# Optimization experiments

Measured on AMD Instinct MI355X. Metric: run time of the kernel, lower is better.

## Reference

```python
import jax, jax.numpy as jnp
import numpy as np

N_NODES = 50000
N_EDGES = 800000
N_REL = 6
N_LAYERS = 8
D = 256
NUM_GRAPHS = 512


def setup_inputs() -> dict:
    key = jax.random.key(0)
    ks = jax.random.split(key, 24)
    s = lambda *sh: 1.0 / np.sqrt(sh[0])
    inp = {
        "x": jax.random.normal(ks[0], (N_NODES, 13), dtype=jnp.float32),
        "edge_index": jax.random.randint(ks[1], (2, N_EDGES), 0, N_NODES, dtype=jnp.int64),
        "edge_type": jax.random.randint(ks[2], (N_EDGES,), 0, N_REL, dtype=jnp.int64),
        "batch": jnp.sort(jax.random.randint(ks[3], (N_NODES,), 0, NUM_GRAPHS, dtype=jnp.int64)),
        "enc_W": jax.random.normal(ks[4], (13, D), dtype=jnp.float32) * s(13),
        "enc_b": jnp.zeros((D,), dtype=jnp.float32),
        "prelu_a": jnp.float32(0.25),
        "rel_W": jax.random.normal(ks[5], (N_LAYERS, N_REL, D, D), dtype=jnp.float32) * s(D),
        "root_W": jax.random.normal(ks[6], (N_LAYERS, D, D), dtype=jnp.float32) * s(D),
        "conv_b": jnp.zeros((N_LAYERS, D), dtype=jnp.float32),
        "gp_W1": jax.random.normal(ks[7], (D, D), dtype=jnp.float32) * s(D),
        "gp_b1": jnp.zeros((D,), dtype=jnp.float32),
        "gp_W2": jax.random.normal(ks[8], (D, D), dtype=jnp.float32) * s(D),
        "gp_b2": jnp.zeros((D,), dtype=jnp.float32),
        "fc_W1": jax.random.normal(ks[9], (D, 1024), dtype=jnp.float32) * s(D),
        "fc_b1": jnp.zeros((1024,), dtype=jnp.float32),
        "fc_W2": jax.random.normal(ks[10], (1024, 512), dtype=jnp.float32) * s(1024),
        "fc_b2": jnp.zeros((512,), dtype=jnp.float32),
        "out_W": jax.random.normal(ks[11], (512, 1), dtype=jnp.float32) * s(512),
        "out_b": jnp.zeros((1,), dtype=jnp.float32),
    }
    return inp


def reference(x, edge_index, edge_type, batch, enc_W, enc_b, prelu_a, rel_W, root_W,
              conv_b, gp_W1, gp_b1, gp_W2, gp_b2, fc_W1, fc_b1, fc_W2, fc_b2, out_W, out_b):
    src, dst = edge_index[0], edge_index[1]
    h = x @ enc_W + enc_b  # [N, D]
    for i in range(N_LAYERS):
        skip = h
        # per-relation transform for all nodes: [R, N, D]
        xW = jnp.einsum('nd,rde->rne', h, rel_W[i])
        msgs = xW[edge_type, src]  # [E, D] gather by (relation, source node)
        agg = jax.ops.segment_sum(msgs, dst, num_segments=N_NODES)
        h = agg + h @ root_W[i] + conv_b[i]
        h = h + skip
        h = jnp.where(h > 0, h, prelu_a * h)  # PReLU (shared scalar)
        norm = jnp.sqrt(jnp.sum(h * h, axis=1, keepdims=True))
        h = h / jnp.maximum(norm, 1e-12)  # F.normalize(p=2, dim=1)
    g = jax.nn.relu(h @ gp_W1 + gp_b1) @ gp_W2 + gp_b2
    pooled = jax.ops.segment_sum(g, batch, num_segments=NUM_GRAPHS)  # global_add_pool
    z = jax.nn.relu(pooled @ fc_W1 + fc_b1)  # dropout = identity at eval
    z = jax.nn.relu(z @ fc_W2 + fc_b2)
    return jax.nn.relu(z @ out_W + out_b)  # [NUM_GRAPHS, 1]
```

## Files before the change

kernel.cpp:

```cpp
#include <hip/hip_runtime.h>

#define N_NODES   50000
#define N_EDGES   800000
#define N_REL     6
#define N_LAYERS  8
#define DD        256
#define NUM_GRAPHS 512

#define NKEYS      (N_REL * N_NODES)
#define SCAN_T     256
#define SCAN_E     8
#define SCAN_CHUNK (SCAN_T * SCAN_E)
#define SCAN_NB    ((NKEYS + SCAN_CHUNK - 1) / SCAN_CHUNK)

typedef _Float16 h4 __attribute__((ext_vector_type(4)));
typedef _Float16 h8 __attribute__((ext_vector_type(8)));
typedef float    f4 __attribute__((ext_vector_type(4)));

__device__ __forceinline__ void atomAddF(float* p, float v) { unsafeAtomicAdd(p, v); }

__device__ __forceinline__ void load_lds16(const void* g, void* l) {
    __builtin_amdgcn_global_load_lds(
        (const __attribute__((address_space(1))) uint32_t*)g,
        (__attribute__((address_space(3))) uint32_t*)l, 16, 0, 0);
}

__global__ __launch_bounds__(256) void enc_kernel(const float* __restrict__ x,
                                                  const float* __restrict__ W,
                                                  const float* __restrict__ b,
                                                  _Float16* __restrict__ Hhi,
                                                  _Float16* __restrict__ Hlo) {
    int n = blockIdx.x;
    int d = threadIdx.x;
    float s = b[d];
#pragma unroll
    for (int k = 0; k < 13; ++k) s = fmaf(x[n * 13 + k], W[k * 256 + d], s);
    const _Float16 hi = (_Float16)s;
    Hhi[(size_t)n * DD + d] = hi;
    Hlo[(size_t)n * DD + d] = (_Float16)(s - (float)hi);
}

__global__ __launch_bounds__(256) void wsplit_rel_kernel(const float* __restrict__ relW,
                                                         const float* __restrict__ rootW,
                                                         _Float16* __restrict__ wthi,
                                                         _Float16* __restrict__ wtlo) {
    const size_t id = (size_t)blockIdx.x * 256 + threadIdx.x;
    if (id >= (size_t)N_LAYERS * 7 * 256 * 256) return;
    const int k = (int)(id & 255);
    const int n = (int)((id >> 8) & 255);
    const int g = (int)((id >> 16) % 7);
    const int L = (int)((id >> 16) / 7);
    float w = (g < 6)
        ? relW[(((size_t)L * 6 + g) * 256 + k) * 256 + n]
        : rootW[((size_t)L * 256 + k) * 256 + n];
    if (g == 6 && k == n) w += 1.0f;
    const _Float16 hi = (_Float16)w;
    const size_t o = ((size_t)L * 256 + n) * 1792 + (size_t)g * 256 + k;
    wthi[o] = hi;
    wtlo[o] = (_Float16)(w - (float)hi);
}

__global__ __launch_bounds__(256) void wsplit_tr_kernel(const float* __restrict__ W,
                                                        _Float16* __restrict__ whi,
                                                        _Float16* __restrict__ wlo,
                                                        int K, int N) {
    const size_t id = (size_t)blockIdx.x * 256 + threadIdx.x;
    if (id >= (size_t)K * N) return;
    const int k = (int)(id % K), n = (int)(id / K);
    const float w = W[(size_t)k * N + n];
    const _Float16 hi = (_Float16)w;
    whi[(size_t)n * K + k] = hi;
    wlo[(size_t)n * K + k] = (_Float16)(w - (float)hi);
}

__global__ __launch_bounds__(256) void fsplit_kernel(const float* __restrict__ S,
                                                     _Float16* __restrict__ hi,
                                                     _Float16* __restrict__ lo, int total) {
    const int id = blockIdx.x * 256 + threadIdx.x;
    if (id >= total) return;
    const float v = S[id];
    const _Float16 h = (_Float16)v;
    hi[id] = h;
    lo[id] = (_Float16)(v - (float)h);
}

__global__ __launch_bounds__(256, 2) void layer_kernel(
    const _Float16* __restrict__ Hhi, const _Float16* __restrict__ Hlo,
    const _Float16* __restrict__ Bhi, const _Float16* __restrict__ Blo,
    const int* __restrict__ ioff, const int* __restrict__ isrc,
    _Float16* __restrict__ Hnhi, _Float16* __restrict__ Hnlo,
    const float* __restrict__ bias, const float* __restrict__ pa) {
    __shared__ _Float16 smem[24576];
    const int tid  = threadIdx.x;
    const int lane = tid & 63;
    const int wave = tid >> 6;
    const int lm = lane & 15, lq = lane >> 4;
    const int wm = wave & 1, wn = wave >> 1;
    const int mb = blockIdx.x * 128;

    const int nl   = tid >> 1;
    const int half = tid & 1;
    const int node = min(mb + nl, N_NODES - 1);

    f4 acc[4][8];
#pragma unroll
    for (int i = 0; i < 4; ++i)
#pragma unroll
        for (int j = 0; j < 8; ++j) acc[i][j] = (f4){0.f, 0.f, 0.f, 0.f};

    for (int seg = 0; seg < 7; ++seg) {
        const bool isrel = (seg < 6);
        int s0 = 0, s1 = 0;
        if (isrel) {
            s0 = ioff[seg * N_NODES + node];
            s1 = ioff[seg * N_NODES + node + 1];
        }
#pragma unroll 1
        for (int c8 = 0; c8 < 8; ++c8) {
            const int acol = c8 * 32;
            const int bcol = seg * 256 + acol;

            __syncthreads();

            if (isrel) {
                float afp[16];
#pragma unroll
                for (int j = 0; j < 16; ++j) afp[j] = 0.f;
                const int dbase = acol + half * 16;
                for (int e = s0; e < s1; ++e) {
                    const int s = isrc[e];
                    const size_t hb = (size_t)s * DD + dbase;
                    const h8 vh0 = *(const h8*)(Hhi + hb);
                    const h8 vh1 = *(const h8*)(Hhi + hb + 8);
                    const h8 vl0 = *(const h8*)(Hlo + hb);
                    const h8 vl1 = *(const h8*)(Hlo + hb + 8);
#pragma unroll
                    for (int j = 0; j < 8; ++j) {
                        afp[j]     += (float)vh0[j] + (float)vl0[j];
                        afp[8 + j] += (float)vh1[j] + (float)vl1[j];
                    }
                }
#pragma unroll
                for (int u = 0; u < 2; ++u) {
                    h8 oh, ol;
#pragma unroll
                    for (int j = 0; j < 8; ++j) {
                        const float v = afp[u * 8 + j];
                        oh[j] = (_Float16)v;
                        ol[j] = (_Float16)(v - (float)oh[j]);
                    }
                    const int cc   = half * 2 + u;
                    const int slot = cc ^ ((nl >> 1) & 3);
                    const int o    = (nl * 4 + slot) * 8;
                    *(h8*)(smem + o)        = oh;
                    *(h8*)(smem + 4096 + o) = ol;
                }
#pragma unroll
                for (int q = 4; q < 12; ++q) {
                    const int ub = (q * 4 + wave) * 64;
                    const int u  = (ub + lane) & 1023;
                    const int row = u >> 2, slot = u & 3;
                    const int cx = slot ^ ((row >> 1) & 3);
                    const _Float16* gp = (q < 8) ? Bhi : Blo;
                    const size_t gb = (size_t)row * 1792 + bcol + cx * 8;
                    load_lds16(gp + gb, smem + (size_t)ub * 8);
                }
            } else {
#pragma unroll
                for (int q = 0; q < 12; ++q) {
                    const int ub = (q * 4 + wave) * 64;
                    const int u  = ub + lane;
                    const _Float16* gp;
                    size_t ga;
                    if (q < 4) {
                        const int v = u & 511, row = v >> 2, slot = v & 3;
                        const int cx = slot ^ ((row >> 1) & 3);
                        const int rg = min(mb + row, N_NODES - 1);
                        gp = (q < 2) ? Hhi : Hlo;
                        ga = (size_t)rg * DD + acol + cx * 8;
                    } else {
                        const int v = u & 1023, row = v >> 2, slot = v & 3;
                        const int cx = slot ^ ((row >> 1) & 3);
                        gp = (q < 8) ? Bhi : Blo;
                        ga = (size_t)row * 1792 + bcol + cx * 8;
                    }
                    load_lds16(gp + ga, smem + (size_t)ub * 8);
                }
            }
            __syncthreads();

            h8 ah[4], al[4], bh[8], bl[8];
#pragma unroll
            for (int i = 0; i < 4; ++i) {
                const int row  = wm * 64 + i * 16 + lm;
                const int slot = lq ^ ((row >> 1) & 3);
                const int o    = (row * 4 + slot) * 8;
                ah[i] = *(const h8*)(smem + o);
                al[i] = *(const h8*)(smem + 4096 + o);
            }
#pragma unroll
            for (int j = 0; j < 8; ++j) {
                const int n    = wn * 128 + j * 16 + lm;
                const int slot = lq ^ ((n >> 1) & 3);
                const int o    = (n * 4 + slot) * 8;
                bh[j] = *(const h8*)(smem + 8192 + o);
                bl[j] = *(const h8*)(smem + 16384 + o);
            }
#pragma unroll
            for (int i = 0; i < 4; ++i)
#pragma unroll
                for (int j = 0; j < 8; ++j) {
                    acc[i][j] = __builtin_amdgcn_mfma_f32_16x16x32_f16(ah[i], bh[j], acc[i][j], 0, 0, 0);
                    acc[i][j] = __builtin_amdgcn_mfma_f32_16x16x32_f16(ah[i], bl[j], acc[i][j], 0, 0, 0);
                    acc[i][j] = __builtin_amdgcn_mfma_f32_16x16x32_f16(al[i], bh[j], acc[i][j], 0, 0, 0);
                }
        }
    }

    float* shf = (float*)smem;
    const float a = pa[0];
    __syncthreads();
#pragma unroll
    for (int i = 0; i < 4; ++i)
#pragma unroll
        for (int r = 0; r < 4; ++r) {
            const int rl  = i * 16 + lq * 4 + r;
            const int row = mb + wm * 64 + rl;
            float rss = 0.f;
            if (row < N_NODES) {
#pragma unroll
                for (int j = 0; j < 8; ++j) {
                    const int col = wn * 128 + j * 16 + lm;
                    float v = acc[i][j][r] + bias[col];
                    v = v > 0.f ? v : a * v;
                    acc[i][j][r] = v;
                    rss = fmaf(v, v, rss);
                }
            }
            rss += __shfl_xor(rss, 1, 64);
            rss += __shfl_xor(rss, 2, 64);
            rss += __shfl_xor(rss, 4, 64);
            rss += __shfl_xor(rss, 8, 64);
            if (lm == 0 && row < N_NODES) shf[wave * 64 + rl] = rss;
        }
    __syncthreads();
#pragma unroll
    for (int i = 0; i < 4; ++i)
#pragma unroll
        for (int r = 0; r < 4; ++r) {
            const int rl  = i * 16 + lq * 4 + r;
            const int row = mb + wm * 64 + rl;
            if (row >= N_NODES) continue;
            const float tot = shf[wm * 64 + rl] + shf[(2 + wm) * 64 + rl];
            const float inv = 1.0f / fmaxf(sqrtf(tot), 1e-12f);
#pragma unroll
            for (int j = 0; j < 8; ++j) {
                const int col = wn * 128 + j * 16 + lm;
                const float v = acc[i][j][r] * inv;
                const _Float16 hi = (_Float16)v;
                const size_t idx = (size_t)row * DD + col;
                Hnhi[idx] = hi;
                Hnlo[idx] = (_Float16)(v - (float)hi);
            }
        }
}

template <int MODE>
__global__ __launch_bounds__(256, 2) void gemm_lds(
    const _Float16* __restrict__ Ahi, const _Float16* __restrict__ Alo,
    const _Float16* __restrict__ Bhi, const _Float16* __restrict__ Blo,
    int lda, int ldb, int ldc, int K_tot,
    _Float16* __restrict__ Ohi, _Float16* __restrict__ Olo,
    const float* __restrict__ bias, int M) {
    __shared__ _Float16 smem[24576];
    const int lane = threadIdx.x & 63;
    const int wave = threadIdx.x >> 6;
    const int lm = lane & 15, lq = lane >> 4;
    const int wm = wave & 1, wn = wave >> 1;
    const int mb = blockIdx.x * 128;
    const int nb = blockIdx.y * 256;

    f4 acc[4][8];
#pragma unroll
    for (int i = 0; i < 4; ++i)
#pragma unroll
        for (int j = 0; j < 8; ++j) acc[i][j] = (f4){0.f, 0.f, 0.f, 0.f};

    for (int k0 = 0; k0 < K_tot; k0 += 32) {
        __syncthreads();
#pragma unroll
        for (int q = 0; q < 12; ++q) {
            const int ub = (q * 4 + wave) * 64;
            const int u  = ub + lane;
            const _Float16* gp;
            size_t ga;
            if (q < 4) {
                const int v = u & 511, row = v >> 2, slot = v & 3;
                const int cx = slot ^ ((row >> 1) & 3);
                const int rg = min(mb + row, M - 1);
                gp = (q < 2) ? Ahi : Alo;
                ga = (size_t)rg * lda + k0 + cx * 8;
            } else {
                const int v = u & 1023, row = v >> 2, slot = v & 3;
                const int cx = slot ^ ((row >> 1) & 3);
                gp = (q < 8) ? Bhi : Blo;
                ga = (size_t)(nb + row) * ldb + k0 + cx * 8;
            }
            load_lds16(gp + ga, smem + (size_t)ub * 8);
        }
        __syncthreads();

        h8 ah[4], al[4], bh[8], bl[8];
#pragma unroll
        for (int i = 0; i < 4; ++i) {
            const int row  = wm * 64 + i * 16 + lm;
            const int slot = lq ^ ((row >> 1) & 3);
            const int o    = (row * 4 + slot) * 8;
            ah[i] = *(const h8*)(smem + o);
            al[i] = *(const h8*)(smem + 4096 + o);
        }
#pragma unroll
        for (int j = 0; j < 8; ++j) {
            const int n    = wn * 128 + j * 16 + lm;
            const int slot = lq ^ ((n >> 1) & 3);
            const int o    = (n * 4 + slot) * 8;
            bh[j] = *(const h8*)(smem + 8192 + o);
            bl[j] = *(const h8*)(smem + 16384 + o);
        }
#pragma unroll
        for (int i = 0; i < 4; ++i)
#pragma unroll
            for (int j = 0; j < 8; ++j) {
                acc[i][j] = __builtin_amdgcn_mfma_f32_16x16x32_f16(ah[i], bh[j], acc[i][j], 0, 0, 0);
                acc[i][j] = __builtin_amdgcn_mfma_f32_16x16x32_f16(ah[i], bl[j], acc[i][j], 0, 0, 0);
                acc[i][j] = __builtin_amdgcn_mfma_f32_16x16x32_f16(al[i], bh[j], acc[i][j], 0, 0, 0);
            }
    }

#pragma unroll
    for (int i = 0; i < 4; ++i)
#pragma unroll
        for (int r = 0; r < 4; ++r) {
            const int row = mb + wm * 64 + i * 16 + lq * 4 + r;
            if (row >= M) continue;
#pragma unroll
            for (int j = 0; j < 8; ++j) {
                const int col = nb + wn * 128 + j * 16 + lm;
                float v = acc[i][j][r] + bias[col];
                if (MODE == 2) v = fmaxf(v, 0.f);
                const _Float16 hi = (_Float16)v;
                const size_t idx = (size_t)row * ldc + col;
                Ohi[idx] = hi;
                Olo[idx] = (_Float16)(v - (float)hi);
            }
        }
}

__global__ __launch_bounds__(256) void hist_kernel(const int* __restrict__ dst,
                                                   const int* __restrict__ etype,
                                                   int* __restrict__ cnt) {
    const int e = blockIdx.x * 256 + threadIdx.x;
    if (e >= N_EDGES) return;
    atomicAdd(&cnt[etype[e] * N_NODES + dst[e]], 1);
}

__global__ __launch_bounds__(SCAN_T) void scan1_kernel(const int* __restrict__ cnt,
                                                       int* __restrict__ off,
                                                       int* __restrict__ bsum) {
    __shared__ int sh[SCAN_T];
    const int b = blockIdx.x, t = threadIdx.x;
    const int base = b * SCAN_CHUNK + t * SCAN_E;
    int pre[SCAN_E];
    int s = 0;
#pragma unroll
    for (int i = 0; i < SCAN_E; ++i) {
        const int x = (base + i < NKEYS) ? cnt[base + i] : 0;
        pre[i] = s;
        s += x;
    }
    sh[t] = s;
    __syncthreads();
    for (int d = 1; d < SCAN_T; d <<= 1) {
        const int x = (t >= d) ? sh[t - d] : 0;
        __syncthreads();
        sh[t] += x;
        __syncthreads();
    }
    const int toff = (t == 0) ? 0 : sh[t - 1];
#pragma unroll
    for (int i = 0; i < SCAN_E; ++i)
        if (base + i < NKEYS) off[base + i] = toff + pre[i];
    if (t == SCAN_T - 1) bsum[b] = sh[SCAN_T - 1];
}

__global__ __launch_bounds__(SCAN_T) void scan2_kernel(int* __restrict__ bsum, int n) {
    __shared__ int sh[SCAN_T];
    const int t = threadIdx.x;
    const int base = t * SCAN_E;
    int pre[SCAN_E];
    int s = 0;
#pragma unroll
    for (int i = 0; i < SCAN_E; ++i) {
        const int x = (base + i < n) ? bsum[base + i] : 0;
        pre[i] = s;
        s += x;
    }
    sh[t] = s;
    __syncthreads();
    for (int d = 1; d < SCAN_T; d <<= 1) {
        const int x = (t >= d) ? sh[t - d] : 0;
        __syncthreads();
        sh[t] += x;
        __syncthreads();
    }
    const int toff = (t == 0) ? 0 : sh[t - 1];
#pragma unroll
    for (int i = 0; i < SCAN_E; ++i)
        if (base + i < n) bsum[base + i] = toff + pre[i];
}

__global__ __launch_bounds__(SCAN_T) void scan3_kernel(int* __restrict__ off,
                                                       const int* __restrict__ bsum) {
    const int b = blockIdx.x, t = threadIdx.x;
    const int add = bsum[b];
    const int base = b * SCAN_CHUNK + t * SCAN_E;
#pragma unroll
    for (int i = 0; i < SCAN_E; ++i)
        if (base + i < NKEYS) off[base + i] += add;
    if (b == 0 && t == 0) off[NKEYS] = N_EDGES;
}

__global__ __launch_bounds__(256) void csr_fill_kernel(const int* __restrict__ src,
                                                       const int* __restrict__ dst,
                                                       const int* __restrict__ etype,
                                                       int* __restrict__ cursor,
                                                       int* __restrict__ sorted_src) {
    const int e = blockIdx.x * 256 + threadIdx.x;
    if (e >= N_EDGES) return;
    const int key = etype[e] * N_NODES + dst[e];
    const int pos = atomicAdd(&cursor[key], 1);
    sorted_src[pos] = src[e];
}

__global__ __launch_bounds__(64) void pool_kernel(const _Float16* __restrict__ ghi,
                                                  const _Float16* __restrict__ glo,
                                                  const int* __restrict__ batch,
                                                  float* __restrict__ pooled) {
    const int c     = threadIdx.x;
    const int start = blockIdx.x * 128;
    const int end   = min(start + 128, N_NODES);
    int cur = batch[start];
    float4 acc = {0.f, 0.f, 0.f, 0.f};
    for (int n = start; n < end; ++n) {
        const int bn = batch[n];
        if (bn != cur) {
            float* p = pooled + (size_t)cur * DD + c * 4;
            atomAddF(p + 0, acc.x); atomAddF(p + 1, acc.y);
            atomAddF(p + 2, acc.z); atomAddF(p + 3, acc.w);
            acc = {0.f, 0.f, 0.f, 0.f};
            cur = bn;
        }
        const h4 vh = *(const h4*)(ghi + (size_t)n * DD + c * 4);
        const h4 vl = *(const h4*)(glo + (size_t)n * DD + c * 4);
        acc.x += (float)vh[0] + (float)vl[0];
        acc.y += (float)vh[1] + (float)vl[1];
        acc.z += (float)vh[2] + (float)vl[2];
        acc.w += (float)vh[3] + (float)vl[3];
    }
    float* p = pooled + (size_t)cur * DD + c * 4;
    atomAddF(p + 0, acc.x); atomAddF(p + 1, acc.y);
    atomAddF(p + 2, acc.z); atomAddF(p + 3, acc.w);
}

__global__ __launch_bounds__(64) void out_kernel(const _Float16* __restrict__ z2hi,
                                                 const _Float16* __restrict__ z2lo,
                                                 const float* __restrict__ W,
                                                 const float* __restrict__ b,
                                                 float* __restrict__ out) {
    const int g = blockIdx.x;
    const int t = threadIdx.x;
    float s = 0.f;
#pragma unroll
    for (int j = 0; j < 8; ++j) {
        const int idx = t + 64 * j;
        const float z = (float)z2hi[(size_t)g * 512 + idx] + (float)z2lo[(size_t)g * 512 + idx];
        s = fmaf(z, W[idx], s);
    }
#pragma unroll
    for (int off = 32; off; off >>= 1) s += __shfl_xor(s, off, 64);
    if (t == 0) {
        const float v = s + b[0];
        out[g] = v > 0.f ? v : 0.f;
    }
}

extern "C" void kernel_launch(void* const* d_in, const int* in_sizes, int n_in,
                              void* d_out, int out_size, void* d_ws, size_t ws_size,
                              hipStream_t stream) {
    const float* x       = (const float*)d_in[0];
    const int*   eidx    = (const int*)d_in[1];
    const int*   etype   = (const int*)d_in[2];
    const int*   batch   = (const int*)d_in[3];
    const float* enc_W   = (const float*)d_in[4];
    const float* enc_b   = (const float*)d_in[5];
    const float* prelu_a = (const float*)d_in[6];
    const float* rel_W   = (const float*)d_in[7];
    const float* root_W  = (const float*)d_in[8];
    const float* conv_b  = (const float*)d_in[9];
    const float* gp_W1   = (const float*)d_in[10];
    const float* gp_b1   = (const float*)d_in[11];
    const float* gp_W2   = (const float*)d_in[12];
    const float* gp_b2   = (const float*)d_in[13];
    const float* fc_W1   = (const float*)d_in[14];
    const float* fc_b1   = (const float*)d_in[15];
    const float* fc_W2   = (const float*)d_in[16];
    const float* fc_b2   = (const float*)d_in[17];
    const float* out_W   = (const float*)d_in[18];
    const float* out_b   = (const float*)d_in[19];
    float* out = (float*)d_out;

    uint8_t* wp = (uint8_t*)d_ws;
    auto alloc = [&](size_t bytes) {
        void* r = (void*)wp;
        wp += (bytes + 255) & ~(size_t)255;
        return r;
    };
    _Float16* H0hi   = (_Float16*)alloc((size_t)N_NODES * DD * 2);
    _Float16* H0lo   = (_Float16*)alloc((size_t)N_NODES * DD * 2);
    _Float16* H1hi   = (_Float16*)alloc((size_t)N_NODES * DD * 2);
    _Float16* H1lo   = (_Float16*)alloc((size_t)N_NODES * DD * 2);
    _Float16* g2hi   = (_Float16*)alloc((size_t)N_NODES * DD * 2);
    _Float16* g2lo   = (_Float16*)alloc((size_t)N_NODES * DD * 2);
    _Float16* wthi   = (_Float16*)alloc((size_t)N_LAYERS * 256 * 1792 * 2);
    _Float16* wtlo   = (_Float16*)alloc((size_t)N_LAYERS * 256 * 1792 * 2);
    _Float16* wtg1hi = (_Float16*)alloc((size_t)256 * 256 * 2);
    _Float16* wtg1lo = (_Float16*)alloc((size_t)256 * 256 * 2);
    _Float16* wtg2hi = (_Float16*)alloc((size_t)256 * 256 * 2);
    _Float16* wtg2lo = (_Float16*)alloc((size_t)256 * 256 * 2);
    _Float16* wtf1hi = (_Float16*)alloc((size_t)1024 * 256 * 2);
    _Float16* wtf1lo = (_Float16*)alloc((size_t)1024 * 256 * 2);
    _Float16* wtf2hi = (_Float16*)alloc((size_t)512 * 1024 * 2);
    _Float16* wtf2lo = (_Float16*)alloc((size_t)512 * 1024 * 2);
    float*    pooled = (float*)alloc((size_t)NUM_GRAPHS * DD * 4);
    _Float16* phi    = (_Float16*)alloc((size_t)NUM_GRAPHS * DD * 2);
    _Float16* plo    = (_Float16*)alloc((size_t)NUM_GRAPHS * DD * 2);
    _Float16* z1hi   = (_Float16*)alloc((size_t)NUM_GRAPHS * 1024 * 2);
    _Float16* z1lo   = (_Float16*)alloc((size_t)NUM_GRAPHS * 1024 * 2);
    _Float16* z2hi   = (_Float16*)alloc((size_t)NUM_GRAPHS * 512 * 2);
    _Float16* z2lo   = (_Float16*)alloc((size_t)NUM_GRAPHS * 512 * 2);
    int*      ioff   = (int*)alloc((size_t)(NKEYS + 1) * 4);
    int*      icur   = (int*)alloc((size_t)NKEYS * 4);
    int*      ibsum  = (int*)alloc(256 * 4);
    int*      isrc   = (int*)alloc((size_t)N_EDGES * 4);

    const int* src = eidx;
    const int* dst = eidx + N_EDGES;

    const size_t wtot = (size_t)N_LAYERS * 7 * 256 * 256;
    wsplit_rel_kernel<<<(int)((wtot + 255) / 256), 256, 0, stream>>>(rel_W, root_W, wthi, wtlo);
    wsplit_tr_kernel<<<256, 256, 0, stream>>>(gp_W1, wtg1hi, wtg1lo, 256, 256);
    wsplit_tr_kernel<<<256, 256, 0, stream>>>(gp_W2, wtg2hi, wtg2lo, 256, 256);
    wsplit_tr_kernel<<<1024, 256, 0, stream>>>(fc_W1, wtf1hi, wtf1lo, 256, 1024);
    wsplit_tr_kernel<<<2048, 256, 0, stream>>>(fc_W2, wtf2hi, wtf2lo, 1024, 512);

    hipMemsetAsync(icur, 0, (size_t)NKEYS * sizeof(int), stream);
    const int eb = (N_EDGES + 255) / 256;
    hist_kernel<<<eb, 256, 0, stream>>>(dst, etype, icur);
    scan1_kernel<<<SCAN_NB, SCAN_T, 0, stream>>>(icur, ioff, ibsum);
    scan2_kernel<<<1, SCAN_T, 0, stream>>>(ibsum, SCAN_NB);
    scan3_kernel<<<SCAN_NB, SCAN_T, 0, stream>>>(ioff, ibsum);
    hipMemcpyAsync(icur, ioff, (size_t)NKEYS * sizeof(int), hipMemcpyDeviceToDevice, stream);
    csr_fill_kernel<<<eb, 256, 0, stream>>>(src, dst, etype, icur, isrc);

    enc_kernel<<<N_NODES, 256, 0, stream>>>(x, enc_W, enc_b, H0hi, H0lo);

    const int gB = (N_NODES + 127) / 128;
    _Float16 *curhi = H0hi, *curlo = H0lo, *nxthi = H1hi, *nxtlo = H1lo;
    for (int L = 0; L < N_LAYERS; ++L) {
        layer_kernel<<<gB, 256, 0, stream>>>(
            curhi, curlo,
            wthi + (size_t)L * 256 * 1792, wtlo + (size_t)L * 256 * 1792,
            ioff, isrc, nxthi, nxtlo, conv_b + L * DD, prelu_a);
        _Float16* t;
        t = curhi; curhi = nxthi; nxthi = t;
        t = curlo; curlo = nxtlo; nxtlo = t;
    }

    gemm_lds<2><<<dim3(gB, 1), 256, 0, stream>>>(curhi, curlo, wtg1hi, wtg1lo,
                                                 256, 256, 256, 256,
                                                 nxthi, nxtlo, gp_b1, N_NODES);
    gemm_lds<4><<<dim3(gB, 1), 256, 0, stream>>>(nxthi, nxtlo, wtg2hi, wtg2lo,
                                                 256, 256, 256, 256,
                                                 g2hi, g2lo, gp_b2, N_NODES);

    hipMemsetAsync(pooled, 0, (size_t)NUM_GRAPHS * DD * sizeof(float), stream);
    pool_kernel<<<(N_NODES + 127) / 128, 64, 0, stream>>>(g2hi, g2lo, batch, pooled);
    fsplit_kernel<<<(NUM_GRAPHS * DD + 255) / 256, 256, 0, stream>>>(
        pooled, phi, plo, NUM_GRAPHS * DD);

    gemm_lds<2><<<dim3(4, 4), 256, 0, stream>>>(phi, plo, wtf1hi, wtf1lo,
                                                256, 256, 1024, 256,
                                                z1hi, z1lo, fc_b1, NUM_GRAPHS);
    gemm_lds<2><<<dim3(4, 2), 256, 0, stream>>>(z1hi, z1lo, wtf2hi, wtf2lo,
                                                1024, 1024, 512, 1024,
                                                z2hi, z2lo, fc_b2, NUM_GRAPHS);
    out_kernel<<<NUM_GRAPHS, 64, 0, stream>>>(z2hi, z2lo, out_W, out_b, out);
}
```

Measured before the change: 3.965 ms.

## Split layer into per-relation GEMM steps overlapped with next-relation aggregation

Replaces the monolithic per-layer kernel, which gathered neighbor features inside the GEMM loop, with a dedicated warp-per-node aggregation pass that writes the pre-aggregated relation input. A chain of fused launches follows, each running the GEMM for one relation while extra blocks aggregate the next relation. A float accumulator buffer carries partial results between launches, and the last step applies the residual, PReLU and normalization. This removes redundant gather work that was repeated per 32-column chunk in the GEMM loop, at the cost of more launches and an extra fp32 read-modify-write of the full node matrix per relation.

```diff
diff --git a/kernel.cpp b/kernel.cpp
--- a/kernel.cpp
+++ b/kernel.cpp
@@ -12,6 +12,9 @@
 #define SCAN_E     8
 #define SCAN_CHUNK (SCAN_T * SCAN_E)
 #define SCAN_NB    ((NKEYS + SCAN_CHUNK - 1) / SCAN_CHUNK)
+
+#define GEMM_B     ((N_NODES + 127) / 128)
+#define AGG_B      ((N_NODES + 3) / 4)
 
 typedef _Float16 h4 __attribute__((ext_vector_type(4)));
 typedef _Float16 h8 __attribute__((ext_vector_type(8)));
@@ -84,185 +87,256 @@
     lo[id] = (_Float16)(v - (float)h);
 }
 
-__global__ __launch_bounds__(256, 2) void layer_kernel(
+__global__ __launch_bounds__(256) void agg1_kernel(const _Float16* __restrict__ Hhi,
+                                                   const _Float16* __restrict__ Hlo,
+                                                   const int* __restrict__ ioff,
+                                                   const int* __restrict__ isrc,
+                                                   _Float16* __restrict__ Phi,
+                                                   _Float16* __restrict__ Plo, int rel) {
+    const int p    = blockIdx.x * 4 + (threadIdx.x >> 6);
+    const int lane = threadIdx.x & 63;
+    const int half = lane >> 5, li = lane & 31;
+    if (p >= N_NODES) return;
+    const int s0 = ioff[rel * N_NODES + p];
+    const int s1 = ioff[rel * N_NODES + p + 1];
+    float a[8] = {0.f, 0.f, 0.f, 0.f, 0.f, 0.f, 0.f, 0.f};
+    for (int e0 = s0; e0 < s1; e0 += 4) {
+        const int ea = e0 + half;
+        const int eb = e0 + 2 + half;
+        const int sa = (ea < s1) ? isrc[ea] : -1;
+        const int sb = (eb < s1) ? isrc[eb] : -1;
+        if (sa >= 0) {
+            const h8 vh = *(const h8*)(Hhi + (size_t)sa * DD + li * 8);
+            const h8 vl = *(const h8*)(Hlo + (size_t)sa * DD + li * 8);
+#pragma unroll
+            for (int k = 0; k < 8; ++k) a[k] += (float)vh[k] + (float)vl[k];
+        }
+        if (sb >= 0) {
+            const h8 vh = *(const h8*)(Hhi + (size_t)sb * DD + li * 8);
+            const h8 vl = *(const h8*)(Hlo + (size_t)sb * DD + li * 8);
+#pragma unroll
+            for (int k = 0; k < 8; ++k) a[k] += (float)vh[k] + (float)vl[k];
+        }
+    }
+#pragma unroll
+    for (int k = 0; k < 8; ++k) a[k] += __shfl_xor(a[k], 32, 64);
+    if (half == 0) {
+        h8 oh, ol;
+#pragma unroll
+        for (int k = 0; k < 8; ++k) {
+            oh[k] = (_Float16)a[k];
+            ol[k] = (_Float16)(a[k] - (float)oh[k]);
+        }
+        const size_t o = (size_t)p * DD + li * 8;
+        *(h8*)(Phi + o) = oh;
+        *(h8*)(Plo + o) = ol;
+    }
+}
+
+template <int MODE, int HAS_AGG>
+__global__ __launch_bounds__(256, 2) void fused_step(
+    const _Float16* __restrict__ Ahi, const _Float16* __restrict__ Alo,
     const _Float16* __restrict__ Hhi, const _Float16* __restrict__ Hlo,
     const _Float16* __restrict__ Bhi, const _Float16* __restrict__ Blo,
-    const int* __restrict__ ioff, const int* __restrict__ isrc,
-    _Float16* __restrict__ Hnhi, _Float16* __restrict__ Hnlo,
-    const float* __restrict__ bias, const float* __restrict__ pa) {
+    int boff_agg, int boff_h, int K_agg, int K_tot,
+    float* __restrict__ Cf, _Float16* __restrict__ Ohi, _Float16* __restrict__ Olo,
+    const float* __restrict__ bias, const float* __restrict__ pa,
+    const int* __restrict__ ioff, const int* __restrict__ isrc, int aggrel,
+    _Float16* __restrict__ Phi, _Float16* __restrict__ Plo) {
     __shared__ _Float16 smem[24576];
-    const int tid  = threadIdx.x;
+    const int tid = threadIdx.x;
+
+    if (HAS_AGG && (int)blockIdx.x >= GEMM_B) {
+        const int p    = ((int)blockIdx.x - GEMM_B) * 4 + (tid >> 6);
+        const int lane = tid & 63;
+        const int half = lane >> 5, li = lane & 31;
+        if (p >= N_NODES) return;
+        const int s0 = ioff[aggrel * N_NODES + p];
+        const int s1 = ioff[aggrel * N_NODES + p + 1];
+        float a[8] = {0.f, 0.f, 0.f, 0.f, 0.f, 0.f, 0.f, 0.f};
+        for (int e0 = s0; e0 < s1; e0 += 4) {
+            const int ea = e0 + half;
+            const int eb = e0 + 2 + half;
+            const int sa = (ea < s1) ? isrc[ea] : -1;
+            const int sb = (eb < s1) ? isrc[eb] : -1;
+            if (sa >= 0) {
+                const h8 vh = *(const h8*)(Hhi + (size_t)sa * DD + li * 8);
+                const h8 vl = *(const h8*)(Hlo + (size_t)sa * DD + li * 8);
+#pragma unroll
+                for (int k = 0; k < 8; ++k) a[k] += (float)vh[k] + (float)vl[k];
+            }
+            if (sb >= 0) {
+                const h8 vh = *(const h8*)(Hhi + (size_t)sb * DD + li * 8);
+                const h8 vl = *(const h8*)(Hlo + (size_t)sb * DD + li * 8);
+#pragma unroll
+                for (int k = 0; k < 8; ++k) a[k] += (float)vh[k] + (float)vl[k];
+            }
+        }
+#pragma unroll
+        for (int k = 0; k < 8; ++k) a[k] += __shfl_xor(a[k], 32, 64);
+        if (half == 0) {
+            h8 oh, ol;
+#pragma unroll
+            for (int k = 0; k < 8; ++k) {
+                oh[k] = (_Float16)a[k];
+                ol[k] = (_Float16)(a[k] - (float)oh[k]);
+            }
+            const size_t o = (size_t)p * DD + li * 8;
+            *(h8*)(Phi + o) = oh;
+            *(h8*)(Plo + o) = ol;
+        }
+        return;
+    }
+
     const int lane = tid & 63;
     const int wave = tid >> 6;
     const int lm = lane & 15, lq = lane >> 4;
     const int wm = wave & 1, wn = wave >> 1;
     const int mb = blockIdx.x * 128;
 
-    const int nl   = tid >> 1;
-    const int half = tid & 1;
-    const int node = min(mb + nl, N_NODES - 1);
-
     f4 acc[4][8];
 #pragma unroll
     for (int i = 0; i < 4; ++i)
 #pragma unroll
         for (int j = 0; j < 8; ++j) acc[i][j] = (f4){0.f, 0.f, 0.f, 0.f};
 
-    for (int seg = 0; seg < 7; ++seg) {
-        const bool isrel = (seg < 6);
-        int s0 = 0, s1 = 0;
-        if (isrel) {
-            s0 = ioff[seg * N_NODES + node];
-            s1 = ioff[seg * N_NODES + node + 1];
-        }
-#pragma unroll 1
-        for (int c8 = 0; c8 < 8; ++c8) {
-            const int acol = c8 * 32;
-            const int bcol = seg * 256 + acol;
-
-            __syncthreads();
-
-            if (isrel) {
-                float afp[16];
-#pragma unroll
-                for (int j = 0; j < 16; ++j) afp[j] = 0.f;
-                const int dbase = acol + half * 16;
-                for (int e = s0; e < s1; ++e) {
-                    const int s = isrc[e];
-                    const size_t hb = (size_t)s * DD + dbase;
-                    const h8 vh0 = *(const h8*)(Hhi + hb);
-                    const h8 vh1 = *(const h8*)(Hhi + hb + 8);
-                    const h8 vl0 = *(const h8*)(Hlo + hb);
-                    const h8 vl1 = *(const h8*)(Hlo + hb + 8);
+    for (int k0 = 0; k0 < K_tot; k0 += 32) {
+        const _Float16 *pAh, *pAl;
+        int acol, bcol;
+        if (k0 < K_agg) {
+            pAh = Ahi; pAl = Alo;
+            acol = k0;
+            bcol = boff_agg + k0;
+        } else {
+            pAh = Hhi; pAl = Hlo;
+            acol = k0 - K_agg;
+            bcol = boff_h + (k0 - K_agg);
+        }
+
+        __syncthreads();
+#pragma unroll
+        for (int q = 0; q < 12; ++q) {
+            const int ub = (q * 4 + wave) * 64;
+            const int u  = ub + lane;
+            const _Float16* gp;
+            size_t ga;
+            if (q < 4) {
+                const int v = u & 511, row = v >> 2, slot = v & 3;
+                const int cx = slot ^ ((row >> 1) & 3);
+                const int rg = min(mb + row, N_NODES - 1);
+                gp = (q < 2) ? pAh : pAl;
+                ga = (size_t)rg * DD + acol + cx * 8;
+            } else {
+                const int v = u & 1023, row = v >> 2, slot = v & 3;
+                const int cx = slot ^ ((row >> 1) & 3);
+                gp = (q < 8) ? Bhi : Blo;
+                ga = (size_t)row * 1792 + bcol + cx * 8;
+            }
+            load_lds16(gp + ga, smem + (size_t)ub * 8);
+        }
+        __syncthreads();
+
+        h8 ah[4], al[4], bh[8], bl[8];
+#pragma unroll
+        for (int i = 0; i < 4; ++i) {
+            const int row  = wm * 64 + i * 16 + lm;
+            const int slot = lq ^ ((row >> 1) & 3);
+            const int o    = (row * 4 + slot) * 8;
+            ah[i] = *(const h8*)(smem + o);
+            al[i] = *(const h8*)(smem + 4096 + o);
+        }
+#pragma unroll
+        for (int j = 0; j < 8; ++j) {
+            const int n    = wn * 128 + j * 16 + lm;
+            const int slot = lq ^ ((n >> 1) & 3);
+            const int o    = (n * 4 + slot) * 8;
+            bh[j] = *(const h8*)(smem + 8192 + o);
+            bl[j] = *(const h8*)(smem + 16384 + o);
+        }
+#pragma unroll
+        for (int i = 0; i < 4; ++i)
+#pragma unroll
+            for (int j = 0; j < 8; ++j) {
+                acc[i][j] = __builtin_amdgcn_mfma_f32_16x16x32_f16(ah[i], bh[j], acc[i][j], 0, 0, 0);
+                acc[i][j] = __builtin_amdgcn_mfma_f32_16x16x32_f16(ah[i], bl[j], acc[i][j], 0, 0, 0);
+                acc[i][j] = __builtin_amdgcn_mfma_f32_16x16x32_f16(al[i], bh[j], acc[i][j], 0, 0, 0);
+            }
+    }
+
+    if (MODE == 0) {
+#pragma unroll
+        for (int i = 0; i < 4; ++i)
+#pragma unroll
+            for (int r = 0; r < 4; ++r) {
+                const int row = mb + wm * 64 + i * 16 + lq * 4 + r;
+                if (row >= N_NODES) continue;
+#pragma unroll
+                for (int j = 0; j < 8; ++j) {
+                    const int col = wn * 128 + j * 16 + lm;
+                    Cf[(size_t)row * DD + col] = acc[i][j][r] + bias[col];
+                }
+            }
+    } else if (MODE == 3) {
+#pragma unroll
+        for (int i = 0; i < 4; ++i)
+#pragma unroll
+            for (int r = 0; r < 4; ++r) {
+                const int row = mb + wm * 64 + i * 16 + lq * 4 + r;
+                if (row >= N_NODES) continue;
+#pragma unroll
+                for (int j = 0; j < 8; ++j) {
+                    const int col = wn * 128 + j * 16 + lm;
+                    Cf[(size_t)row * DD + col] += acc[i][j][r];
+                }
+            }
+    } else {
+        float* shf = (float*)smem;
+        const float a = pa[0];
+        __syncthreads();
+#pragma unroll
+        for (int i = 0; i < 4; ++i)
+#pragma unroll
+            for (int r = 0; r < 4; ++r) {
+                const int rl  = i * 16 + lq * 4 + r;
+                const int row = mb + wm * 64 + rl;
+                float rss = 0.f;
+                if (row < N_NODES) {
 #pragma unroll
                     for (int j = 0; j < 8; ++j) {
-                        afp[j]     += (float)vh0[j] + (float)vl0[j];
-                        afp[8 + j] += (float)vh1[j] + (float)vl1[j];
+                        const int col = wn * 128 + j * 16 + lm;
+                        float v = acc[i][j][r] + Cf[(size_t)row * DD + col];
+                        v = v > 0.f ? v : a * v;
+                        acc[i][j][r] = v;
+                        rss = fmaf(v, v, rss);
                     }
                 }
-#pragma unroll
-                for (int u = 0; u < 2; ++u) {
-                    h8 oh, ol;
-#pragma unroll
-                    for (int j = 0; j < 8; ++j) {
-                        const float v = afp[u * 8 + j];
-                        oh[j] = (_Float16)v;
-                        ol[j] = (_Float16)(v - (float)oh[j]);
-                    }
-                    const int cc   = half * 2 + u;
-                    const int slot = cc ^ ((nl >> 1) & 3);
-                    const int o    = (nl * 4 + slot) * 8;
-                    *(h8*)(smem + o)        = oh;
-                    *(h8*)(smem + 4096 + o) = ol;
-                }
-#pragma unroll
-                for (int q = 4; q < 12; ++q) {
-                    const int ub = (q * 4 + wave) * 64;
-                    const int u  = (ub + lane) & 1023;
-                    const int row = u >> 2, slot = u & 3;
-                    const int cx = slot ^ ((row >> 1) & 3);
-                    const _Float16* gp = (q < 8) ? Bhi : Blo;
-                    const size_t gb = (size_t)row * 1792 + bcol + cx * 8;
-                    load_lds16(gp + gb, smem + (size_t)ub * 8);
-                }
-            } else {
-#pragma unroll
-                for (int q = 0; q < 12; ++q) {
-                    const int ub = (q * 4 + wave) * 64;
-                    const int u  = ub + lane;
-                    const _Float16* gp;
-                    size_t ga;
-                    if (q < 4) {
-                        const int v = u & 511, row = v >> 2, slot = v & 3;
-                        const int cx = slot ^ ((row >> 1) & 3);
-                        const int rg = min(mb + row, N_NODES - 1);
-                        gp = (q < 2) ? Hhi : Hlo;
-                        ga = (size_t)rg * DD + acol + cx * 8;
-                    } else {
-                        const int v = u & 1023, row = v >> 2, slot = v & 3;
-                        const int cx = slot ^ ((row >> 1) & 3);
-                        gp = (q < 8) ? Bhi : Blo;
-                        ga = (size_t)row * 1792 + bcol + cx * 8;
-                    }
-                    load_lds16(gp + ga, smem + (size_t)ub * 8);
-                }
-            }
-            __syncthreads();
-
-            h8 ah[4], al[4], bh[8], bl[8];
-#pragma unroll
-            for (int i = 0; i < 4; ++i) {
-                const int row  = wm * 64 + i * 16 + lm;
-                const int slot = lq ^ ((row >> 1) & 3);
-                const int o    = (row * 4 + slot) * 8;
-                ah[i] = *(const h8*)(smem + o);
-                al[i] = *(const h8*)(smem + 4096 + o);
-            }
-#pragma unroll
-            for (int j = 0; j < 8; ++j) {
-                const int n    = wn * 128 + j * 16 + lm;
-                const int slot = lq ^ ((n >> 1) & 3);
-                const int o    = (n * 4 + slot) * 8;
-                bh[j] = *(const h8*)(smem + 8192 + o);
-                bl[j] = *(const h8*)(smem + 16384 + o);
-            }
-#pragma unroll
-            for (int i = 0; i < 4; ++i)
-#pragma unroll
-                for (int j = 0; j < 8; ++j) {
-                    acc[i][j] = __builtin_amdgcn_mfma_f32_16x16x32_f16(ah[i], bh[j], acc[i][j], 0, 0, 0);
-                    acc[i][j] = __builtin_amdgcn_mfma_f32_16x16x32_f16(ah[i], bl[j], acc[i][j], 0, 0, 0);
-                    acc[i][j] = __builtin_amdgcn_mfma_f32_16x16x32_f16(al[i], bh[j], acc[i][j], 0, 0, 0);
-                }
-        }
-    }
-
-    float* shf = (float*)smem;
-    const float a = pa[0];
-    __syncthreads();
-#pragma unroll
-    for (int i = 0; i < 4; ++i)
-#pragma unroll
-        for (int r = 0; r < 4; ++r) {
-            const int rl  = i * 16 + lq * 4 + r;
-            const int row = mb + wm * 64 + rl;
-            float rss = 0.f;
-            if (row < N_NODES) {
+                rss += __shfl_xor(rss, 1, 64);
+                rss += __shfl_xor(rss, 2, 64);
+                rss += __shfl_xor(rss, 4, 64);
+                rss += __shfl_xor(rss, 8, 64);
+                if (lm == 0 && row < N_NODES) shf[wave * 64 + rl] = rss;
+            }
+        __syncthreads();
+#pragma unroll
+        for (int i = 0; i < 4; ++i)
+#pragma unroll
+            for (int r = 0; r < 4; ++r) {
+                const int rl  = i * 16 + lq * 4 + r;
+                const int row = mb + wm * 64 + rl;
+                if (row >= N_NODES) continue;
+                const float tot = shf[wm * 64 + rl] + shf[(2 + wm) * 64 + rl];
+                const float inv = 1.0f / fmaxf(sqrtf(tot), 1e-12f);
 #pragma unroll
                 for (int j = 0; j < 8; ++j) {
                     const int col = wn * 128 + j * 16 + lm;
-                    float v = acc[i][j][r] + bias[col];
-                    v = v > 0.f ? v : a * v;
-                    acc[i][j][r] = v;
-                    rss = fmaf(v, v, rss);
+                    const float v = acc[i][j][r] * inv;
+                    const _Float16 hi = (_Float16)v;
+                    const size_t idx = (size_t)row * DD + col;
+                    Ohi[idx] = hi;
+                    Olo[idx] = (_Float16)(v - (float)hi);
                 }
             }
-            rss += __shfl_xor(rss, 1, 64);
-            rss += __shfl_xor(rss, 2, 64);
-            rss += __shfl_xor(rss, 4, 64);
-            rss += __shfl_xor(rss, 8, 64);
-            if (lm == 0 && row < N_NODES) shf[wave * 64 + rl] = rss;
-        }
-    __syncthreads();
-#pragma unroll
-    for (int i = 0; i < 4; ++i)
-#pragma unroll
-        for (int r = 0; r < 4; ++r) {
-            const int rl  = i * 16 + lq * 4 + r;
-            const int row = mb + wm * 64 + rl;
-            if (row >= N_NODES) continue;
-            const float tot = shf[wm * 64 + rl] + shf[(2 + wm) * 64 + rl];
-            const float inv = 1.0f / fmaxf(sqrtf(tot), 1e-12f);
-#pragma unroll
-            for (int j = 0; j < 8; ++j) {
-                const int col = wn * 128 + j * 16 + lm;
-                const float v = acc[i][j][r] * inv;
-                const _Float16 hi = (_Float16)v;
-                const size_t idx = (size_t)row * DD + col;
-                Hnhi[idx] = hi;
-                Hnlo[idx] = (_Float16)(v - (float)hi);
-            }
-        }
+    }
 }
 
 template <int MODE>
@@ -525,12 +599,13 @@
         wp += (bytes + 255) & ~(size_t)255;
         return r;
     };
-    _Float16* H0hi   = (_Float16*)alloc((size_t)N_NODES * DD * 2);
-    _Float16* H0lo   = (_Float16*)alloc((size_t)N_NODES * DD * 2);
-    _Float16* H1hi   = (_Float16*)alloc((size_t)N_NODES * DD * 2);
-    _Float16* H1lo   = (_Float16*)alloc((size_t)N_NODES * DD * 2);
-    _Float16* g2hi   = (_Float16*)alloc((size_t)N_NODES * DD * 2);
-    _Float16* g2lo   = (_Float16*)alloc((size_t)N_NODES * DD * 2);
+    _Float16* Hhi    = (_Float16*)alloc((size_t)N_NODES * DD * 2);
+    _Float16* Hlo    = (_Float16*)alloc((size_t)N_NODES * DD * 2);
+    float*    base   = (float*)alloc((size_t)N_NODES * DD * 4);
+    _Float16* P0hi   = (_Float16*)alloc((size_t)N_NODES * DD * 2);
+    _Float16* P0lo   = (_Float16*)alloc((size_t)N_NODES * DD * 2);
+    _Float16* P1hi   = (_Float16*)alloc((size_t)N_NODES * DD * 2);
+    _Float16* P1lo   = (_Float16*)alloc((size_t)N_NODES * DD * 2);
     _Float16* wthi   = (_Float16*)alloc((size_t)N_LAYERS * 256 * 1792 * 2);
     _Float16* wtlo   = (_Float16*)alloc((size_t)N_LAYERS * 256 * 1792 * 2);
     _Float16* wtg1hi = (_Float16*)alloc((size_t)256 * 256 * 2);
@@ -572,29 +647,52 @@
     hipMemcpyAsync(icur, ioff, (size_t)NKEYS * sizeof(int), hipMemcpyDeviceToDevice, stream);
     csr_fill_kernel<<<eb, 256, 0, stream>>>(src, dst, etype, icur, isrc);
 
-    enc_kernel<<<N_NODES, 256, 0, stream>>>(x, enc_W, enc_b, H0hi, H0lo);
-
-    const int gB = (N_NODES + 127) / 128;
-    _Float16 *curhi = H0hi, *curlo = H0lo, *nxthi = H1hi, *nxtlo = H1lo;
+    enc_kernel<<<N_NODES, 256, 0, stream>>>(x, enc_W, enc_b, Hhi, Hlo);
+    agg1_kernel<<<AGG_B, 256, 0, stream>>>(Hhi, Hlo, ioff, isrc, P0hi, P0lo, 0);
+
+    const dim3 gFat(GEMM_B + AGG_B);
+    const dim3 gG(GEMM_B);
     for (int L = 0; L < N_LAYERS; ++L) {
-        layer_kernel<<<gB, 256, 0, stream>>>(
-            curhi, curlo,
-            wthi + (size_t)L * 256 * 1792, wtlo + (size_t)L * 256 * 1792,
-            ioff, isrc, nxthi, nxtlo, conv_b + L * DD, prelu_a);
-        _Float16* t;
-        t = curhi; curhi = nxthi; nxthi = t;
-        t = curlo; curlo = nxtlo; nxtlo = t;
-    }
-
-    gemm_lds<2><<<dim3(gB, 1), 256, 0, stream>>>(curhi, curlo, wtg1hi, wtg1lo,
-                                                 256, 256, 256, 256,
-                                                 nxthi, nxtlo, gp_b1, N_NODES);
-    gemm_lds<4><<<dim3(gB, 1), 256, 0, stream>>>(nxthi, nxtlo, wtg2hi, wtg2lo,
-                                                 256, 256, 256, 256,
-                                                 g2hi, g2lo, gp_b2, N_NODES);
+        const _Float16* Bh = wthi + (size_t)L * 256 * 1792;
+        const _Float16* Bl = wtlo + (size_t)L * 256 * 1792;
+        const float*    cb = conv_b + L * DD;
+        fused_step<0, 1><<<gFat, 256, 0, stream>>>(
+            P0hi, P0lo, Hhi, Hlo, Bh, Bl, 0, 1536, 256, 512,
+            base, nullptr, nullptr, cb, nullptr,
+            ioff, isrc, 1, P1hi, P1lo);
+        fused_step<3, 1><<<gFat, 256, 0, stream>>>(
+            P1hi, P1lo, Hhi, Hlo, Bh, Bl, 256, 0, 256, 256,
+            base, nullptr, nullptr, nullptr, nullptr,
+            ioff, isrc, 2, P0hi, P0lo);
+        fused_step<3, 1><<<gFat, 256, 0, stream>>>(
+            P0hi, P0lo, Hhi, Hlo, Bh, Bl, 512, 0, 256, 256,
+            base, nullptr, nullptr, nullptr, nullptr,
+            ioff, isrc, 3, P1hi, P1lo);
+        fused_step<3, 1><<<gFat, 256, 0, stream>>>(
+            P1hi, P1lo, Hhi, Hlo, Bh, Bl, 768, 0, 256, 256,
+            base, nullptr, nullptr, nullptr, nullptr,
+            ioff, isrc, 4, P0hi, P0lo);
+        fused_step<3, 1><<<gFat, 256, 0, stream>>>(
+            P0hi, P0lo, Hhi, Hlo, Bh, Bl, 1024, 0, 256, 256,
+            base, nullptr, nullptr, nullptr, nullptr,
+            ioff, isrc, 5, P1hi, P1lo);
+        fused_step<1, 0><<<gG, 256, 0, stream>>>(
+            P1hi, P1lo, Hhi, Hlo, Bh, Bl, 1280, 0, 256, 256,
+            base, Hhi, Hlo, nullptr, prelu_a,
+            nullptr, nullptr, 0, nullptr, nullptr);
+        if (L < N_LAYERS - 1)
+            agg1_kernel<<<AGG_B, 256, 0, stream>>>(Hhi, Hlo, ioff, isrc, P0hi, P0lo, 0);
+    }
+
+    gemm_lds<2><<<dim3(GEMM_B, 1), 256, 0, stream>>>(Hhi, Hlo, wtg1hi, wtg1lo,
+                                                     256, 256, 256, 256,
+                                                     P0hi, P0lo, gp_b1, N_NODES);
+    gemm_lds<4><<<dim3(GEMM_B, 1), 256, 0, stream>>>(P0hi, P0lo, wtg2hi, wtg2lo,
+                                                     256, 256, 256, 256,
+                                                     P1hi, P1lo, gp_b2, N_NODES);
 
     hipMemsetAsync(pooled, 0, (size_t)NUM_GRAPHS * DD * sizeof(float), stream);
-    pool_kernel<<<(N_NODES + 127) / 128, 64, 0, stream>>>(g2hi, g2lo, batch, pooled);
+    pool_kernel<<<(N_NODES + 127) / 128, 64, 0, stream>>>(P1hi, P1lo, batch, pooled);
     fsplit_kernel<<<(NUM_GRAPHS * DD + 255) / 256, 256, 0, stream>>>(
         pooled, phi, plo, NUM_GRAPHS * DD);
 
```

After: 5.069 ms. 1.28x slower.
